# Performance work log

Measured on AMD Instinct MI355X. Metric: run time of the kernel, lower is better.

## Reference

```python
import jax, jax.numpy as jnp
import numpy as np

N = 50000
E = 800000
D = 128


def setup_inputs() -> dict:
    key = jax.random.key(0)
    ks = jax.random.split(key, 10)
    x = jax.random.normal(ks[0], (N, D), dtype=jnp.float32)
    edge_index = jax.random.randint(ks[1], (2, E), 0, N, dtype=jnp.int32)
    s = 1.0 / np.sqrt(D)
    W1 = jax.random.uniform(ks[2], (D, D), jnp.float32, -s, s)
    b1 = jnp.zeros((D,), jnp.float32)
    W2 = jax.random.uniform(ks[3], (D, D), jnp.float32, -s, s)
    b2 = jnp.zeros((D,), jnp.float32)
    Wt = jax.random.uniform(ks[4], (D, 1), jnp.float32, -s, s)
    bt = jnp.zeros((1,), jnp.float32)
    We = jax.random.uniform(ks[5], (D, 1), jnp.float32, -s, s)
    be = jnp.zeros((1,), jnp.float32)
    return {"x": x, "edge_index": edge_index, "W1": W1, "b1": b1,
            "W2": W2, "b2": b2, "Wt": Wt, "bt": bt, "We": We, "be": be}


def _gcn_norm(edge_index, n):
    # add self-loops, then symmetric normalization D^-1/2 (A+I) D^-1/2
    loop = jnp.arange(n, dtype=edge_index.dtype)
    src = jnp.concatenate([edge_index[0], loop])
    dst = jnp.concatenate([edge_index[1], loop])
    ones = jnp.ones(src.shape[0], dtype=jnp.float32)
    deg = jax.ops.segment_sum(ones, dst, num_segments=n)
    dinv = jnp.where(deg > 0, jax.lax.rsqrt(deg), 0.0)
    norm = dinv[src] * dinv[dst]  # [E+N]
    return src, dst, norm


def _gcn_conv(h, W, b, src, dst, norm, n):
    h = h @ W                                   # [N, D'] dense GEMM
    msg = h[src] * norm[:, None]                # gather + scale
    out = jax.ops.segment_sum(msg, dst, num_segments=n)  # scatter-add
    return out + b


def reference(x, edge_index, W1, b1, W2, b2, Wt, bt, We, be):
    n = x.shape[0]
    src, dst, norm = _gcn_norm(edge_index, n)
    h = jax.nn.relu(_gcn_conv(x, W1, b1, src, dst, norm, n))
    h = jax.nn.relu(_gcn_conv(h, W2, b2, src, dst, norm, n))
    # dropout is identity at inference (eval mode)
    survival_time = h @ Wt + bt   # [N, 1]
    event_status = h @ We + be    # [N, 1]
    return survival_time, event_status
```

## Files before the change

### kernel.cpp

```cpp
#include <hip/hip_runtime.h>
#include <hip/hip_fp16.h>
#include <math.h>

#define NN 50000
#define NNP 50048
#define NE 800000
#define DD 128

#define NB  196
#define CAP 5300
#define CAPP 6400
#define EPB 4096
#define A_BLOCKS 196

#define SLAB2 (NNP * 64)

typedef _Float16 half8_t __attribute__((ext_vector_type(8)));
typedef float f32x4 __attribute__((ext_vector_type(4)));


__global__ __launch_bounds__(256) void k_setup(const int* __restrict__ src, const int* __restrict__ dst,
                                               int* __restrict__ bcnt, unsigned int* __restrict__ ebuf,
                                               const float* __restrict__ W1, const float* __restrict__ W2,
                                               __half* __restrict__ WT1, __half* __restrict__ WT2) {
    const int blk = blockIdx.x;
    const int tid = threadIdx.x;

    if (blk < A_BLOCKS) {
        __shared__ int hist[256];
        __shared__ int scanbuf[256];
        __shared__ int gbase[256];
        __shared__ unsigned int stage[EPB];
        __shared__ int tgt[EPB];

        const int e0 = blk * EPB;
        int nE = NE - e0; if (nE > EPB) nE = EPB;

        hist[tid] = 0;
        __syncthreads();

        unsigned int pk[16];
        unsigned int br[16];
        #pragma unroll
        for (int j = 0; j < 16; ++j) {
            int idx = tid + j * 256;
            if (idx < nE) {
                int e = e0 + idx;
                int s = src[e], d = dst[e];
                int b = d >> 8;
                int r = atomicAdd(&hist[b], 1);
                pk[j] = (unsigned int)s | ((unsigned int)(d & 255) << 16);
                br[j] = (unsigned int)b | ((unsigned int)r << 8);
            }
        }
        __syncthreads();
        int v = hist[tid];
        scanbuf[tid] = v;
        __syncthreads();
        for (int o = 1; o < 256; o <<= 1) {
            int t2 = (tid >= o) ? scanbuf[tid - o] : 0;
            __syncthreads();
            scanbuf[tid] += t2;
            __syncthreads();
        }
        int base_excl = scanbuf[tid] - v;
        if (tid < NB && v > 0) gbase[tid] = tid * CAP + atomicAdd(&bcnt[tid], v);
        hist[tid] = base_excl;
        __syncthreads();

        #pragma unroll
        for (int j = 0; j < 16; ++j) {
            int idx = tid + j * 256;
            if (idx < nE) {
                int b = br[j] & 255;
                int r = (int)(br[j] >> 8);
                int pos = hist[b] + r;
                stage[pos] = pk[j];
                tgt[pos]   = gbase[b] + r;
            }
        }
        __syncthreads();
        #pragma unroll
        for (int j = 0; j < 16; ++j) {
            int idx = tid + j * 256;
            if (idx < nE) ebuf[tgt[idx]] = stage[idx];
        }
    } else {
        const float* W  = (blk == A_BLOCKS) ? W1 : W2;
        __half*      WT = (blk == A_BLOCKS) ? WT1 : WT2;
        int n = tid >> 1;
        int k0 = (tid & 1) * 64;
        #pragma unroll 8
        for (int j = 0; j < 64; ++j) {
            int k = k0 + j;
            WT[n * DD + k] = __float2half(W[k * DD + n]);
        }
    }
}


__global__ __launch_bounds__(512) void k_build_csr(const unsigned int* __restrict__ ebuf,
                                                   const int* __restrict__ bcnt,
                                                   int* __restrict__ rowbeg, int* __restrict__ rowend,
                                                   float* __restrict__ dinv,
                                                   unsigned short* __restrict__ col) {
    __shared__ int cnt[256];
    __shared__ int scanb[256];
    __shared__ unsigned short stage[CAPP];

    const int b   = blockIdx.x;
    const int tid = threadIdx.x;
    const int seg0 = b * CAP;
    const int sb   = bcnt[b];
    const int n0   = b << 8;
    int nb = NN - n0; if (nb > 256) nb = 256;

    if (tid < 256) cnt[tid] = 0;
    __syncthreads();
    for (int p = tid; p < sb; p += 512) {
        unsigned int e = ebuf[seg0 + p];
        atomicAdd(&cnt[(e >> 16) & 255], 1);
    }
    __syncthreads();
    int v  = (tid < 256) ? cnt[tid] : 0;
    int pv = (v + 7) & ~7;
    if (tid < 256) scanb[tid] = pv;
    __syncthreads();
    for (int o = 1; o < 256; o <<= 1) {
        int t = 0;
        if (tid < 256 && tid >= o) t = scanb[tid - o];
        __syncthreads();
        if (tid < 256) scanb[tid] += t;
        __syncthreads();
    }
    int exclp = (tid < 256) ? (scanb[tid] - pv) : 0;
    if (tid < nb) {
        rowbeg[n0 + tid] = b * CAPP + exclp;
        rowend[n0 + tid] = b * CAPP + exclp + pv;
        dinv[n0 + tid] = rsqrtf(1.0f + (float)v);
    }
    if (tid < 256) cnt[tid] = exclp;
    __syncthreads();
    for (int p = tid; p < sb; p += 512) {
        unsigned int e = ebuf[seg0 + p];
        int pos = atomicAdd(&cnt[(e >> 16) & 255], 1);
        stage[pos] = (unsigned short)(e & 0xFFFFu);
    }
    __syncthreads();
    if (tid < nb) {
        for (int k = exclp + v; k < exclp + pv; ++k) stage[k] = (unsigned short)NN;
    }
    __syncthreads();
    const int sbp = scanb[255];
    for (int p = tid; p < sbp; p += 512) {
        col[b * CAPP + p] = stage[p];
    }
}


#define LPAD 136
#define GEMM_B 782
#define ZERO_B 98

__global__ __launch_bounds__(256) void k_gemm_x(const float* __restrict__ X, const __half* __restrict__ WT,
                                                const float* __restrict__ dinv, __half* __restrict__ Gc,
                                                float* __restrict__ zbuf, int zcount) {
    const int tid = threadIdx.x;

    if (blockIdx.x >= GEMM_B) {
        int idx = (blockIdx.x - GEMM_B) * 256 + tid;
        if (idx * 4 + 3 < zcount) ((float4*)zbuf)[idx] = make_float4(0.f, 0.f, 0.f, 0.f);
        else {
            for (int k = idx * 4; k < zcount; ++k) zbuf[k] = 0.f;
        }
        return;
    }

    __shared__ __half Wl[DD * LPAD];
    __shared__ __half Al[64 * LPAD];

    const int row0 = blockIdx.x * 64;

    {
        const uint4* WTg = (const uint4*)WT;
        #pragma unroll
        for (int j = 0; j < 8; ++j) {
            int u = tid + j * 256;
            int n = u >> 4, koff = (u & 15) * 8;
            uint4 v = WTg[u];
            *(uint4*)&Wl[n * LPAD + koff] = v;
        }
    }
    {
        const float4* X4 = (const float4*)X;
        #pragma unroll
        for (int j = 0; j < 8; ++j) {
            int u = tid + j * 256;
            int r = u >> 5, c4 = u & 31;
            int grow = row0 + r;
            float4 v = make_float4(0.f, 0.f, 0.f, 0.f);
            if (grow < NN) v = X4[(size_t)grow * 32 + c4];
            __half2 a = __floats2half2_rn(v.x, v.y);
            __half2 b = __floats2half2_rn(v.z, v.w);
            uint2 pk;
            pk.x = *(unsigned int*)&a;
            pk.y = *(unsigned int*)&b;
            *(uint2*)&Al[r * LPAD + c4 * 4] = pk;
        }
    }
    __syncthreads();

    const int wave = tid >> 6;
    const int lane = tid & 63;
    const int m    = lane & 15;
    const int quad = lane >> 4;

    f32x4 acc[8];
    #pragma unroll
    for (int t = 0; t < 8; ++t) acc[t] = (f32x4){0.f, 0.f, 0.f, 0.f};

    #pragma unroll
    for (int kk = 0; kk < DD; kk += 32) {
        half8_t a = *(const half8_t*)&Al[(wave * 16 + m) * LPAD + kk + quad * 8];
        #pragma unroll
        for (int t = 0; t < 8; ++t) {
            half8_t b = *(const half8_t*)&Wl[(t * 16 + m) * LPAD + kk + quad * 8];
            acc[t] = __builtin_amdgcn_mfma_f32_16x16x32_f16(a, b, acc[t], 0, 0, 0);
        }
    }

    __syncthreads();

    float4 dv = *(const float4*)&dinv[row0 + wave * 16 + quad * 4];

    #pragma unroll
    for (int t = 0; t < 8; ++t) {
        #pragma unroll
        for (int r = 0; r < 4; ++r) {
            int row_l = wave * 16 + quad * 4 + r;
            int c     = t * 16 + m;
            float val = acc[t][r] * ((const float*)&dv)[r];
            Al[row_l * LPAD + c] = __float2half(val);
        }
    }
    __syncthreads();

    {
        #pragma unroll
        for (int j = 0; j < 4; ++j) {
            int u = tid + j * 256;
            int r = u >> 4, c16 = u & 15;
            int ch = c16 >> 3, wi = c16 & 7;
            int grow = row0 + r;
            uint4 v = *(const uint4*)&Al[r * LPAD + c16 * 8];
            *(uint4*)(Gc + (size_t)ch * SLAB2 + (size_t)grow * 64 + wi * 8) = v;
        }
    }
}


__global__ __launch_bounds__(256) void k_gemm_h(const __half* __restrict__ Xc, const __half* __restrict__ WT,
                                                __half* __restrict__ Gc) {
    __shared__ __half Wl[DD * LPAD];
    __shared__ __half Al[64 * LPAD];

    const int tid  = threadIdx.x;
    const int row0 = blockIdx.x * 64;

    {
        const uint4* WTg = (const uint4*)WT;
        #pragma unroll
        for (int j = 0; j < 8; ++j) {
            int u = tid + j * 256;
            int n = u >> 4, koff = (u & 15) * 8;
            uint4 v = WTg[u];
            *(uint4*)&Wl[n * LPAD + koff] = v;
        }
    }
    {
        #pragma unroll
        for (int j = 0; j < 4; ++j) {
            int u = tid + j * 256;
            int r = u >> 4, c16 = u & 15;
            int ch = c16 >> 3, wi = c16 & 7;
            int grow = row0 + r;
            uint4 v;
            if (grow < NN) v = *(const uint4*)(Xc + (size_t)ch * SLAB2 + (size_t)grow * 64 + wi * 8);
            else { v.x = 0; v.y = 0; v.z = 0; v.w = 0; }
            *(uint4*)&Al[r * LPAD + c16 * 8] = v;
        }
    }
    __syncthreads();

    const int wave = tid >> 6;
    const int lane = tid & 63;
    const int m    = lane & 15;
    const int quad = lane >> 4;

    f32x4 acc[8];
    #pragma unroll
    for (int t = 0; t < 8; ++t) acc[t] = (f32x4){0.f, 0.f, 0.f, 0.f};

    #pragma unroll
    for (int kk = 0; kk < DD; kk += 32) {
        half8_t a = *(const half8_t*)&Al[(wave * 16 + m) * LPAD + kk + quad * 8];
        #pragma unroll
        for (int t = 0; t < 8; ++t) {
            half8_t b = *(const half8_t*)&Wl[(t * 16 + m) * LPAD + kk + quad * 8];
            acc[t] = __builtin_amdgcn_mfma_f32_16x16x32_f16(a, b, acc[t], 0, 0, 0);
        }
    }

    __syncthreads();

    #pragma unroll
    for (int t = 0; t < 8; ++t) {
        #pragma unroll
        for (int r = 0; r < 4; ++r) {
            int row_l = wave * 16 + quad * 4 + r;
            int c     = t * 16 + m;
            Al[row_l * LPAD + c] = __float2half(acc[t][r]);
        }
    }
    __syncthreads();

    {
        #pragma unroll
        for (int j = 0; j < 4; ++j) {
            int u = tid + j * 256;
            int r = u >> 4, c16 = u & 15;
            int ch = c16 >> 3, wi = c16 & 7;
            int grow = row0 + r;
            uint4 v = *(const uint4*)&Al[r * LPAD + c16 * 8];
            *(uint4*)(Gc + (size_t)ch * SLAB2 + (size_t)grow * 64 + wi * 8) = v;
        }
    }
}


__device__ inline float4 h4_to_f4(uint2 r) {
    __half2 a = *(__half2*)&r.x;
    __half2 b = *(__half2*)&r.y;
    float2 lo = __half22float2(a), hi = __half22float2(b);
    return make_float4(lo.x, lo.y, hi.x, hi.y);
}

__device__ inline uint2 f4_to_h4(float4 v) {
    __half2 a = __floats2half2_rn(v.x, v.y);
    __half2 b = __floats2half2_rn(v.z, v.w);
    uint2 r;
    r.x = *(unsigned int*)&a;
    r.y = *(unsigned int*)&b;
    return r;
}

__device__ inline float4 gather_grp64(const __half* __restrict__ slab, int node, int fl,
                                      const unsigned short* __restrict__ col, int beg, int end) {
    const __half* base = slab + fl * 4;
    float4 accA = h4_to_f4(*(const uint2*)(base + (size_t)node * 64));
    float4 accB = make_float4(0.f, 0.f, 0.f, 0.f);
    for (int p = beg; p < end; p += 8) {
        uint4 c8 = *(const uint4*)(col + p);
        int s0 = c8.x & 0xFFFF, s1 = c8.x >> 16;
        int s2 = c8.y & 0xFFFF, s3 = c8.y >> 16;
        int s4 = c8.z & 0xFFFF, s5 = c8.z >> 16;
        int s6 = c8.w & 0xFFFF, s7 = c8.w >> 16;
        float4 v0 = h4_to_f4(*(const uint2*)(base + (size_t)s0 * 64));
        float4 v1 = h4_to_f4(*(const uint2*)(base + (size_t)s1 * 64));
        float4 v2 = h4_to_f4(*(const uint2*)(base + (size_t)s2 * 64));
        float4 v3 = h4_to_f4(*(const uint2*)(base + (size_t)s3 * 64));
        float4 v4 = h4_to_f4(*(const uint2*)(base + (size_t)s4 * 64));
        float4 v5 = h4_to_f4(*(const uint2*)(base + (size_t)s5 * 64));
        float4 v6 = h4_to_f4(*(const uint2*)(base + (size_t)s6 * 64));
        float4 v7 = h4_to_f4(*(const uint2*)(base + (size_t)s7 * 64));
        accA.x += (v0.x + v1.x) + (v4.x + v5.x);
        accA.y += (v0.y + v1.y) + (v4.y + v5.y);
        accA.z += (v0.z + v1.z) + (v4.z + v5.z);
        accA.w += (v0.w + v1.w) + (v4.w + v5.w);
        accB.x += (v2.x + v3.x) + (v6.x + v7.x);
        accB.y += (v2.y + v3.y) + (v6.y + v7.y);
        accB.z += (v2.z + v3.z) + (v6.z + v7.z);
        accB.w += (v2.w + v3.w) + (v6.w + v7.w);
    }
    accA.x += accB.x; accA.y += accB.y; accA.z += accB.z; accA.w += accB.w;
    return accA;
}

__global__ __launch_bounds__(256) void k_aggregate_c(const __half* __restrict__ G, const float* __restrict__ dinv,
                                                     const int* __restrict__ rowbeg, const int* __restrict__ rowend,
                                                     const unsigned short* __restrict__ col,
                                                     const float* __restrict__ bias, __half* __restrict__ H) {
    const int bx    = blockIdx.x;
    const int slot  = bx & 7;
    const int chunk = slot >> 2;
    const int nb    = (bx >> 3) * 4 + (slot & 3);
    const int g     = threadIdx.x >> 4;
    const int fl    = threadIdx.x & 15;
    const int node  = nb * 16 + g;
    if (node >= NN) return;

    const __half* slab = G + (size_t)chunk * SLAB2;
    int beg = rowbeg[node];
    int end = rowend[node];
    float4 acc = gather_grp64(slab, node, fl, col, beg, end);

    float di = dinv[node];
    float4 bv = *(const float4*)(bias + chunk * 64 + fl * 4);
    float4 hv;
    hv.x = di * fmaxf(fmaf(di, acc.x, bv.x), 0.f);
    hv.y = di * fmaxf(fmaf(di, acc.y, bv.y), 0.f);
    hv.z = di * fmaxf(fmaf(di, acc.z, bv.z), 0.f);
    hv.w = di * fmaxf(fmaf(di, acc.w, bv.w), 0.f);
    *(uint2*)(H + (size_t)chunk * SLAB2 + (size_t)node * 64 + fl * 4) = f4_to_h4(hv);
}

__global__ __launch_bounds__(256) void k_aggregate_heads_c(const __half* __restrict__ G, const float* __restrict__ dinv,
                                                           const int* __restrict__ rowbeg, const int* __restrict__ rowend,
                                                           const unsigned short* __restrict__ col,
                                                           const float* __restrict__ bias,
                                                           const float* __restrict__ Wt, const float* __restrict__ bt,
                                                           const float* __restrict__ We, const float* __restrict__ be,
                                                           float* __restrict__ out) {
    const int bx    = blockIdx.x;
    const int slot  = bx & 7;
    const int chunk = slot >> 2;
    const int nb    = (bx >> 3) * 4 + (slot & 3);
    const int g     = threadIdx.x >> 4;
    const int fl    = threadIdx.x & 15;
    const int node  = nb * 16 + g;
    if (node >= NN) return;

    const __half* slab = G + (size_t)chunk * SLAB2;
    int beg = rowbeg[node];
    int end = rowend[node];
    float4 acc = gather_grp64(slab, node, fl, col, beg, end);

    float di = dinv[node];
    float4 bv = *(const float4*)(bias + chunk * 64 + fl * 4);
    float hx = fmaxf(fmaf(di, acc.x, bv.x), 0.f);
    float hy = fmaxf(fmaf(di, acc.y, bv.y), 0.f);
    float hz = fmaxf(fmaf(di, acc.z, bv.z), 0.f);
    float hw = fmaxf(fmaf(di, acc.w, bv.w), 0.f);

    float4 wt = *(const float4*)(Wt + chunk * 64 + fl * 4);
    float4 we = *(const float4*)(We + chunk * 64 + fl * 4);
    float t  = hx * wt.x + hy * wt.y + hz * wt.z + hw * wt.w;
    float ev = hx * we.x + hy * we.y + hz * we.z + hw * we.w;
    #pragma unroll
    for (int o = 1; o < 16; o <<= 1) {
        t  += __shfl_xor(t, o, 64);
        ev += __shfl_xor(ev, o, 64);
    }
    if (fl == 0) {
        if (chunk == 0) { t += bt[0]; ev += be[0]; }
        atomicAdd(&out[node], t);
        atomicAdd(&out[NN + node], ev);
    }
}


extern "C" void kernel_launch(void* const* d_in, const int* in_sizes, int n_in,
                              void* d_out, int out_size, void* d_ws, size_t ws_size,
                              hipStream_t stream) {
    const float* x  = (const float*)d_in[0];
    const int*   ei = (const int*)d_in[1];
    const float* W1 = (const float*)d_in[2];
    const float* b1 = (const float*)d_in[3];
    const float* W2 = (const float*)d_in[4];
    const float* b2 = (const float*)d_in[5];
    const float* Wt = (const float*)d_in[6];
    const float* bt = (const float*)d_in[7];
    const float* We = (const float*)d_in[8];
    const float* be = (const float*)d_in[9];
    float* out = (float*)d_out;

    const int* srcI = ei;
    const int* dstI = ei + NE;

    char* w = (char*)d_ws;
    __half*         Gh    = (__half*)w;         w += (size_t)2 * SLAB2 * sizeof(__half);
    __half*         H1h   = (__half*)w;         w += (size_t)2 * SLAB2 * sizeof(__half);
    __half*         WT1   = (__half*)w;         w += (size_t)DD * DD * sizeof(__half);
    __half*         WT2   = (__half*)w;         w += (size_t)DD * DD * sizeof(__half);
    unsigned int*   ebuf  = (unsigned int*)w;   w += (size_t)NB * CAP * sizeof(unsigned int);
    unsigned short* col   = (unsigned short*)w; w += (size_t)NB * CAPP * sizeof(unsigned short);
    float*          dinv  = (float*)w;          w += (size_t)(NN + 64) * sizeof(float);
    int*            rowbeg= (int*)w;            w += (size_t)NN * sizeof(int);
    int*            rowend= (int*)w;            w += (size_t)NN * sizeof(int);
    int*            bcnt  = (int*)w;            w += (size_t)NB * sizeof(int);

    const int SETUP_B = A_BLOCKS + 2;
    const int NBLK    = (NN + 15) / 16;
    const int AGG_B   = ((NBLK + 3) / 4) * 8;

    hipMemsetAsync(bcnt, 0, (size_t)NB * sizeof(int), stream);

    hipLaunchKernelGGL(k_setup,     dim3(SETUP_B), dim3(256), 0, stream,
                       srcI, dstI, bcnt, ebuf, W1, W2, WT1, WT2);
    hipLaunchKernelGGL(k_build_csr, dim3(NB),      dim3(512), 0, stream, ebuf, bcnt, rowbeg, rowend, dinv, col);

    hipLaunchKernelGGL(k_gemm_x,      dim3(GEMM_B + ZERO_B), dim3(256), 0, stream, x, WT1, dinv, Gh, out, out_size);
    hipLaunchKernelGGL(k_aggregate_c, dim3(AGG_B),           dim3(256), 0, stream, Gh, dinv, rowbeg, rowend, col, b1, H1h);

    hipLaunchKernelGGL(k_gemm_h,            dim3(GEMM_B), dim3(256), 0, stream, H1h, WT2, Gh);
    hipLaunchKernelGGL(k_aggregate_heads_c, dim3(AGG_B),  dim3(256), 0, stream, Gh, dinv, rowbeg, rowend, col, b2,
                       Wt, bt, We, be, out);
}
```

Before: 184.9 us.

## Replace column-chunked feature slabs with row-major layout and full-row aggregation

Feature buffers move from two 64-column slabs to a single row-major [N,128] fp16 layout, and each node is aggregated by 32 lanes covering the full row instead of two separate blocks each covering half. This removes the atomic accumulation of the output heads and the zero-fill blocks, so outputs are written directly. The trade-off is that each gathered neighbour row spans 256 bytes instead of 128, which changes cache locality: the chunked layout kept each pass's working set to half the feature matrix.

```diff
diff --git a/kernel.cpp b/kernel.cpp
--- a/kernel.cpp
+++ b/kernel.cpp
@@ -12,8 +12,6 @@
 #define CAPP 6400
 #define EPB 4096
 #define A_BLOCKS 196
-
-#define SLAB2 (NNP * 64)
 
 typedef _Float16 half8_t __attribute__((ext_vector_type(8)));
 typedef float f32x4 __attribute__((ext_vector_type(4)));
@@ -160,25 +158,13 @@
 
 #define LPAD 136
 #define GEMM_B 782
-#define ZERO_B 98
 
 __global__ __launch_bounds__(256) void k_gemm_x(const float* __restrict__ X, const __half* __restrict__ WT,
-                                                const float* __restrict__ dinv, __half* __restrict__ Gc,
-                                                float* __restrict__ zbuf, int zcount) {
-    const int tid = threadIdx.x;
-
-    if (blockIdx.x >= GEMM_B) {
-        int idx = (blockIdx.x - GEMM_B) * 256 + tid;
-        if (idx * 4 + 3 < zcount) ((float4*)zbuf)[idx] = make_float4(0.f, 0.f, 0.f, 0.f);
-        else {
-            for (int k = idx * 4; k < zcount; ++k) zbuf[k] = 0.f;
-        }
-        return;
-    }
-
+                                                const float* __restrict__ dinv, __half* __restrict__ Gc) {
     __shared__ __half Wl[DD * LPAD];
     __shared__ __half Al[64 * LPAD];
 
+    const int tid  = threadIdx.x;
     const int row0 = blockIdx.x * 64;
 
     {
@@ -250,10 +236,9 @@
         for (int j = 0; j < 4; ++j) {
             int u = tid + j * 256;
             int r = u >> 4, c16 = u & 15;
-            int ch = c16 >> 3, wi = c16 & 7;
             int grow = row0 + r;
             uint4 v = *(const uint4*)&Al[r * LPAD + c16 * 8];
-            *(uint4*)(Gc + (size_t)ch * SLAB2 + (size_t)grow * 64 + wi * 8) = v;
+            *(uint4*)(Gc + (size_t)grow * DD + c16 * 8) = v;
         }
     }
 }
@@ -282,10 +267,9 @@
         for (int j = 0; j < 4; ++j) {
             int u = tid + j * 256;
             int r = u >> 4, c16 = u & 15;
-            int ch = c16 >> 3, wi = c16 & 7;
             int grow = row0 + r;
             uint4 v;
-            if (grow < NN) v = *(const uint4*)(Xc + (size_t)ch * SLAB2 + (size_t)grow * 64 + wi * 8);
+            if (grow < NN) v = *(const uint4*)(Xc + (size_t)grow * DD + c16 * 8);
             else { v.x = 0; v.y = 0; v.z = 0; v.w = 0; }
             *(uint4*)&Al[r * LPAD + c16 * 8] = v;
         }
@@ -329,10 +313,9 @@
         for (int j = 0; j < 4; ++j) {
             int u = tid + j * 256;
             int r = u >> 4, c16 = u & 15;
-            int ch = c16 >> 3, wi = c16 & 7;
             int grow = row0 + r;
             uint4 v = *(const uint4*)&Al[r * LPAD + c16 * 8];
-            *(uint4*)(Gc + (size_t)ch * SLAB2 + (size_t)grow * 64 + wi * 8) = v;
+            *(uint4*)(Gc + (size_t)grow * DD + c16 * 8) = v;
         }
     }
 }
@@ -354,10 +337,10 @@
     return r;
 }
 
-__device__ inline float4 gather_grp64(const __half* __restrict__ slab, int node, int fl,
-                                      const unsigned short* __restrict__ col, int beg, int end) {
-    const __half* base = slab + fl * 4;
-    float4 accA = h4_to_f4(*(const uint2*)(base + (size_t)node * 64));
+__device__ inline float4 gather_row(const __half* __restrict__ G, int node, int fl,
+                                    const unsigned short* __restrict__ col, int beg, int end) {
+    const __half* base = G + fl * 4;
+    float4 accA = h4_to_f4(*(const uint2*)(base + (size_t)node * DD));
     float4 accB = make_float4(0.f, 0.f, 0.f, 0.f);
     for (int p = beg; p < end; p += 8) {
         uint4 c8 = *(const uint4*)(col + p);
@@ -365,14 +348,14 @@
         int s2 = c8.y & 0xFFFF, s3 = c8.y >> 16;
         int s4 = c8.z & 0xFFFF, s5 = c8.z >> 16;
         int s6 = c8.w & 0xFFFF, s7 = c8.w >> 16;
-        float4 v0 = h4_to_f4(*(const uint2*)(base + (size_t)s0 * 64));
-        float4 v1 = h4_to_f4(*(const uint2*)(base + (size_t)s1 * 64));
-        float4 v2 = h4_to_f4(*(const uint2*)(base + (size_t)s2 * 64));
-        float4 v3 = h4_to_f4(*(const uint2*)(base + (size_t)s3 * 64));
-        float4 v4 = h4_to_f4(*(const uint2*)(base + (size_t)s4 * 64));
-        float4 v5 = h4_to_f4(*(const uint2*)(base + (size_t)s5 * 64));
-        float4 v6 = h4_to_f4(*(const uint2*)(base + (size_t)s6 * 64));
-        float4 v7 = h4_to_f4(*(const uint2*)(base + (size_t)s7 * 64));
+        float4 v0 = h4_to_f4(*(const uint2*)(base + (size_t)s0 * DD));
+        float4 v1 = h4_to_f4(*(const uint2*)(base + (size_t)s1 * DD));
+        float4 v2 = h4_to_f4(*(const uint2*)(base + (size_t)s2 * DD));
+        float4 v3 = h4_to_f4(*(const uint2*)(base + (size_t)s3 * DD));
+        float4 v4 = h4_to_f4(*(const uint2*)(base + (size_t)s4 * DD));
+        float4 v5 = h4_to_f4(*(const uint2*)(base + (size_t)s5 * DD));
+        float4 v6 = h4_to_f4(*(const uint2*)(base + (size_t)s6 * DD));
+        float4 v7 = h4_to_f4(*(const uint2*)(base + (size_t)s7 * DD));
         accA.x += (v0.x + v1.x) + (v4.x + v5.x);
         accA.y += (v0.y + v1.y) + (v4.y + v5.y);
         accA.z += (v0.z + v1.z) + (v4.z + v5.z);
@@ -386,75 +369,62 @@
     return accA;
 }
 
-__global__ __launch_bounds__(256) void k_aggregate_c(const __half* __restrict__ G, const float* __restrict__ dinv,
-                                                     const int* __restrict__ rowbeg, const int* __restrict__ rowend,
-                                                     const unsigned short* __restrict__ col,
-                                                     const float* __restrict__ bias, __half* __restrict__ H) {
-    const int bx    = blockIdx.x;
-    const int slot  = bx & 7;
-    const int chunk = slot >> 2;
-    const int nb    = (bx >> 3) * 4 + (slot & 3);
-    const int g     = threadIdx.x >> 4;
-    const int fl    = threadIdx.x & 15;
-    const int node  = nb * 16 + g;
+__global__ __launch_bounds__(256) void k_aggregate(const __half* __restrict__ G, const float* __restrict__ dinv,
+                                                   const int* __restrict__ rowbeg, const int* __restrict__ rowend,
+                                                   const unsigned short* __restrict__ col,
+                                                   const float* __restrict__ bias, __half* __restrict__ H) {
+    const int node = blockIdx.x * 8 + (threadIdx.x >> 5);
+    const int fl   = threadIdx.x & 31;
     if (node >= NN) return;
 
-    const __half* slab = G + (size_t)chunk * SLAB2;
     int beg = rowbeg[node];
     int end = rowend[node];
-    float4 acc = gather_grp64(slab, node, fl, col, beg, end);
+    float4 acc = gather_row(G, node, fl, col, beg, end);
 
     float di = dinv[node];
-    float4 bv = *(const float4*)(bias + chunk * 64 + fl * 4);
+    float4 bv = ((const float4*)bias)[fl];
     float4 hv;
     hv.x = di * fmaxf(fmaf(di, acc.x, bv.x), 0.f);
     hv.y = di * fmaxf(fmaf(di, acc.y, bv.y), 0.f);
     hv.z = di * fmaxf(fmaf(di, acc.z, bv.z), 0.f);
     hv.w = di * fmaxf(fmaf(di, acc.w, bv.w), 0.f);
-    *(uint2*)(H + (size_t)chunk * SLAB2 + (size_t)node * 64 + fl * 4) = f4_to_h4(hv);
-}
-
-__global__ __launch_bounds__(256) void k_aggregate_heads_c(const __half* __restrict__ G, const float* __restrict__ dinv,
-                                                           const int* __restrict__ rowbeg, const int* __restrict__ rowend,
-                                                           const unsigned short* __restrict__ col,
-                                                           const float* __restrict__ bias,
-                                                           const float* __restrict__ Wt, const float* __restrict__ bt,
-                                                           const float* __restrict__ We, const float* __restrict__ be,
-                                                           float* __restrict__ out) {
-    const int bx    = blockIdx.x;
-    const int slot  = bx & 7;
-    const int chunk = slot >> 2;
-    const int nb    = (bx >> 3) * 4 + (slot & 3);
-    const int g     = threadIdx.x >> 4;
-    const int fl    = threadIdx.x & 15;
-    const int node  = nb * 16 + g;
+    *(uint2*)(H + (size_t)node * DD + fl * 4) = f4_to_h4(hv);
+}
+
+__global__ __launch_bounds__(256) void k_aggregate_heads(const __half* __restrict__ G, const float* __restrict__ dinv,
+                                                         const int* __restrict__ rowbeg, const int* __restrict__ rowend,
+                                                         const unsigned short* __restrict__ col,
+                                                         const float* __restrict__ bias,
+                                                         const float* __restrict__ Wt, const float* __restrict__ bt,
+                                                         const float* __restrict__ We, const float* __restrict__ be,
+                                                         float* __restrict__ out) {
+    const int node = blockIdx.x * 8 + (threadIdx.x >> 5);
+    const int fl   = threadIdx.x & 31;
     if (node >= NN) return;
 
-    const __half* slab = G + (size_t)chunk * SLAB2;
     int beg = rowbeg[node];
     int end = rowend[node];
-    float4 acc = gather_grp64(slab, node, fl, col, beg, end);
+    float4 acc = gather_row(G, node, fl, col, beg, end);
 
     float di = dinv[node];
-    float4 bv = *(const float4*)(bias + chunk * 64 + fl * 4);
+    float4 bv = ((const float4*)bias)[fl];
     float hx = fmaxf(fmaf(di, acc.x, bv.x), 0.f);
     float hy = fmaxf(fmaf(di, acc.y, bv.y), 0.f);
     float hz = fmaxf(fmaf(di, acc.z, bv.z), 0.f);
     float hw = fmaxf(fmaf(di, acc.w, bv.w), 0.f);
 
-    float4 wt = *(const float4*)(Wt + chunk * 64 + fl * 4);
-    float4 we = *(const float4*)(We + chunk * 64 + fl * 4);
+    float4 wt = ((const float4*)Wt)[fl];
+    float4 we = ((const float4*)We)[fl];
     float t  = hx * wt.x + hy * wt.y + hz * wt.z + hw * wt.w;
     float ev = hx * we.x + hy * we.y + hz * we.z + hw * we.w;
     #pragma unroll
-    for (int o = 1; o < 16; o <<= 1) {
+    for (int o = 1; o < 32; o <<= 1) {
         t  += __shfl_xor(t, o, 64);
         ev += __shfl_xor(ev, o, 64);
     }
     if (fl == 0) {
-        if (chunk == 0) { t += bt[0]; ev += be[0]; }
-        atomicAdd(&out[node], t);
-        atomicAdd(&out[NN + node], ev);
+        out[node]      = t + bt[0];
+        out[NN + node] = ev + be[0];
     }
 }
 
@@ -478,8 +448,8 @@
     const int* dstI = ei + NE;
 
     char* w = (char*)d_ws;
-    __half*         Gh    = (__half*)w;         w += (size_t)2 * SLAB2 * sizeof(__half);
-    __half*         H1h   = (__half*)w;         w += (size_t)2 * SLAB2 * sizeof(__half);
+    __half*         Gh    = (__half*)w;         w += (size_t)NNP * DD * sizeof(__half);
+    __half*         H1h   = (__half*)w;         w += (size_t)NNP * DD * sizeof(__half);
     __half*         WT1   = (__half*)w;         w += (size_t)DD * DD * sizeof(__half);
     __half*         WT2   = (__half*)w;         w += (size_t)DD * DD * sizeof(__half);
     unsigned int*   ebuf  = (unsigned int*)w;   w += (size_t)NB * CAP * sizeof(unsigned int);
@@ -490,8 +460,7 @@
     int*            bcnt  = (int*)w;            w += (size_t)NB * sizeof(int);
 
     const int SETUP_B = A_BLOCKS + 2;
-    const int NBLK    = (NN + 15) / 16;
-    const int AGG_B   = ((NBLK + 3) / 4) * 8;
+    const int AGG_B   = (NN + 7) / 8;
 
     hipMemsetAsync(bcnt, 0, (size_t)NB * sizeof(int), stream);
 
@@ -499,10 +468,10 @@
                        srcI, dstI, bcnt, ebuf, W1, W2, WT1, WT2);
     hipLaunchKernelGGL(k_build_csr, dim3(NB),      dim3(512), 0, stream, ebuf, bcnt, rowbeg, rowend, dinv, col);
 
-    hipLaunchKernelGGL(k_gemm_x,      dim3(GEMM_B + ZERO_B), dim3(256), 0, stream, x, WT1, dinv, Gh, out, out_size);
-    hipLaunchKernelGGL(k_aggregate_c, dim3(AGG_B),           dim3(256), 0, stream, Gh, dinv, rowbeg, rowend, col, b1, H1h);
-
-    hipLaunchKernelGGL(k_gemm_h,            dim3(GEMM_B), dim3(256), 0, stream, H1h, WT2, Gh);
-    hipLaunchKernelGGL(k_aggregate_heads_c, dim3(AGG_B),  dim3(256), 0, stream, Gh, dinv, rowbeg, rowend, col, b2,
+    hipLaunchKernelGGL(k_gemm_x,    dim3(GEMM_B), dim3(256), 0, stream, x, WT1, dinv, Gh);
+    hipLaunchKernelGGL(k_aggregate, dim3(AGG_B),  dim3(256), 0, stream, Gh, dinv, rowbeg, rowend, col, b1, H1h);
+
+    hipLaunchKernelGGL(k_gemm_h,          dim3(GEMM_B), dim3(256), 0, stream, H1h, WT2, Gh);
+    hipLaunchKernelGGL(k_aggregate_heads, dim3(AGG_B),  dim3(256), 0, stream, Gh, dinv, rowbeg, rowend, col, b2,
                        Wt, bt, We, be, out);
 }
```

Result: no change. 187.1 us (+1.2%).
